# Performance work log

Measured on AMD Instinct MI355X. Metric: run time of the kernel, lower is better.

Reference implementation:

```python
import jax, jax.numpy as jnp
import numpy as np

B, N, D, P = 8, 256, 1024, 512  # batch, n_words, input_dim, proj_dim


def setup_inputs() -> dict:
    key = jax.random.key(0)
    ks = jax.random.split(key, 8)
    w = lambda k, shape: (jax.random.normal(k, shape, dtype=jnp.float32) * 0.02)
    return {
        "x": jax.random.normal(ks[0], (B, N, D), dtype=jnp.float32),
        # bigram path
        "Wl": w(ks[1], (P, D)), "bl": jnp.zeros((P,), jnp.float32),
        "Wr": w(ks[2], (P, D)),  # right proj has no bias
        "Wo": w(ks[3], (1, P)), "bo": jnp.zeros((1,), jnp.float32),
        # start builder: Linear -> ReLU -> Linear
        "Ws1": w(ks[4], (P, D)), "bs1": jnp.zeros((P,), jnp.float32),
        "Ws2": w(ks[5], (1, P)), "bs2": jnp.zeros((1,), jnp.float32),
        # end builder
        "We1": w(ks[6], (P, D)), "be1": jnp.zeros((P,), jnp.float32),
        "We2": w(ks[7], (1, P)), "be2": jnp.zeros((1,), jnp.float32),
    }


def reference(x, Wl, bl, Wr, Wo, bo, Ws1, bs1, Ws2, bs2, We1, be1, We2, be2):
    # start / end scorers: [B,N,1]
    start = jax.nn.relu(jnp.einsum('bnd,pd->bnp', x, Ws1) + bs1) @ Ws2.T + bs2
    end = jax.nn.relu(jnp.einsum('bnd,pd->bnp', x, We1) + be1) @ We2.T + be2
    # bigram projections: [B,N,P]
    left = jnp.einsum('bnd,pd->bnp', x, Wl) + bl
    right = jnp.einsum('bnd,pd->bnp', x, Wr)
    # outer-sum: proj[b,i,j,:] = left[b,j,:] + right[b,i,:]  -> [B,N,N,P]
    proj = jax.nn.relu(left[:, None, :, :] + right[:, :, None, :])
    bigram = jnp.einsum('bijp,qp->bijq', proj, Wo) + bo  # [B,N,N,1]
    return (bigram, start, end)
```

## Files before the change

kernel.cpp:

```cpp
#include <hip/hip_runtime.h>
#include <hip/hip_fp16.h>

typedef __attribute__((ext_vector_type(8))) short short8;
typedef __attribute__((ext_vector_type(4))) float f32x4;

constexpr int kB = 8;
constexpr int kN = 256;
constexpr int kD = 1024;
constexpr int kP = 512;
constexpr int kM = kB * kN;

__device__ __forceinline__ __half2 pk_max2(__half2 a, __half2 b) {
    unsigned ua = *reinterpret_cast<unsigned*>(&a);
    unsigned ub = *reinterpret_cast<unsigned*>(&b);
    unsigned ur;
    asm("v_pk_max_f16 %0, %1, %2" : "=v"(ur) : "v"(ua), "v"(ub));
    return *reinterpret_cast<__half2*>(&ur);
}

__global__ __launch_bounds__(256) void cvt_kernel(
    const float* __restrict__ x,
    const float* __restrict__ Wl, const float* __restrict__ Wr,
    const float* __restrict__ Ws1, const float* __restrict__ We1,
    const float* __restrict__ bs2, const float* __restrict__ be2,
    unsigned short* __restrict__ xb, unsigned short* __restrict__ wb,
    float* __restrict__ out_start, float* __restrict__ out_end)
{
    const int bid = blockIdx.x;
    if (bid >= 2048) {
        const int idx = (bid - 2048) * 256 + threadIdx.x;
        if (idx < 2048) out_start[idx] = bs2[0];
        else            out_end[idx - 2048] = be2[0];
        return;
    }
    const int g = bid * 256 + threadIdx.x;
    const float* src;
    unsigned short* dst;
    if (g < 262144) {
        src = x + (size_t)g * 8;
        dst = xb + (size_t)g * 8;
    } else {
        const int gg = g - 262144;
        const int w = gg >> 16;
        const int r = gg & 65535;
        const float* s = (w == 0) ? Wl : (w == 1) ? Wr : (w == 2) ? Ws1 : We1;
        src = s + (size_t)r * 8;
        dst = wb + ((size_t)w << 19) + (size_t)r * 8;
    }
    const float4 a = *reinterpret_cast<const float4*>(src);
    const float4 b = *reinterpret_cast<const float4*>(src + 4);
    const float v[8] = {a.x, a.y, a.z, a.w, b.x, b.y, b.z, b.w};
    short8 o;
#pragma unroll
    for (int i = 0; i < 8; ++i) {
        unsigned u = __float_as_uint(v[i]);
        u = u + 0x7FFF + ((u >> 16) & 1);
        o[i] = (short)(u >> 16);
    }
    *reinterpret_cast<short8*>(dst) = o;
}

__global__ __launch_bounds__(512) void proj_mfma(
    const unsigned short* __restrict__ xb, const unsigned short* __restrict__ wb,
    const float* __restrict__ bl, const float* __restrict__ bs1,
    const float* __restrict__ be1,
    const float* __restrict__ Ws2, const float* __restrict__ We2,
    __half* __restrict__ left_h, __half* __restrict__ right_h,
    float* __restrict__ out_start, float* __restrict__ out_end)
{
    __shared__ unsigned short As[2][128 * 64];
    __shared__ unsigned short Bs[2][128 * 64];

    const int L = blockIdx.x;
    const int slot = L >> 3;
    const int by = (L & 7) * 2 + (slot >> 4);
    const int bx = slot & 15;
    const int r0 = bx * 128;
    const int q0 = by * 128;
    const int z  = q0 >> 9;
    const int t = threadIdx.x, wid = t >> 6, lane = t & 63;
    const int wr = wid >> 2, wc = wid & 3;

    f32x4 acc[4][2] = {};

    const int srow0 = wid * 16 + (lane >> 3);
    const int scolh = ((lane & 7) ^ (lane >> 3)) << 3;
    const unsigned short* gA0 = xb + (size_t)(r0 + srow0) * kD + scolh;
    const unsigned short* gA1 = gA0 + (size_t)8 * kD;
    const unsigned short* gB0 = wb + (size_t)(q0 + srow0) * kD + scolh;
    const unsigned short* gB1 = gB0 + (size_t)8 * kD;

#define STAGE(buf, k0) do { \
    __builtin_amdgcn_global_load_lds( \
        (const __attribute__((address_space(1))) void*)(gA0 + (k0)), \
        (__attribute__((address_space(3))) void*)((char*)&As[buf][0] + wid * 2048), 16, 0, 0); \
    __builtin_amdgcn_global_load_lds( \
        (const __attribute__((address_space(1))) void*)(gA1 + (k0)), \
        (__attribute__((address_space(3))) void*)((char*)&As[buf][0] + wid * 2048 + 1024), 16, 0, 0); \
    __builtin_amdgcn_global_load_lds( \
        (const __attribute__((address_space(1))) void*)(gB0 + (k0)), \
        (__attribute__((address_space(3))) void*)((char*)&Bs[buf][0] + wid * 2048), 16, 0, 0); \
    __builtin_amdgcn_global_load_lds( \
        (const __attribute__((address_space(1))) void*)(gB1 + (k0)), \
        (__attribute__((address_space(3))) void*)((char*)&Bs[buf][0] + wid * 2048 + 1024), 16, 0, 0); \
} while (0)

    const int sw = (lane & 7) << 4;
    const int cb0 = (lane >> 4) * 16;
    const int rA = wr * 64 + (lane & 15);
    const int rB = wc * 32 + (lane & 15);

    STAGE(0, 0);
    __syncthreads();
    int cur = 0;
    for (int k0 = 0; k0 < kD; k0 += 64) {
        if (k0 + 64 < kD) STAGE(cur ^ 1, k0 + 64);
        short8 a[4][2], b[2][2];
#pragma unroll
        for (int m = 0; m < 4; ++m)
#pragma unroll
            for (int ks = 0; ks < 2; ++ks)
                a[m][ks] = *reinterpret_cast<const short8*>(
                    (const char*)&As[cur][0] +
                    (rA + m * 16) * 128 + ((ks * 64 + cb0) ^ sw));
#pragma unroll
        for (int n = 0; n < 2; ++n)
#pragma unroll
            for (int ks = 0; ks < 2; ++ks)
                b[n][ks] = *reinterpret_cast<const short8*>(
                    (const char*)&Bs[cur][0] +
                    (rB + n * 16) * 128 + ((ks * 64 + cb0) ^ sw));
#pragma unroll
        for (int m = 0; m < 4; ++m)
#pragma unroll
            for (int n = 0; n < 2; ++n)
#pragma unroll
                for (int ks = 0; ks < 2; ++ks)
                    acc[m][n] = __builtin_amdgcn_mfma_f32_16x16x32_bf16(
                        a[m][ks], b[n][ks], acc[m][n], 0, 0, 0);
        __syncthreads();
        cur ^= 1;
    }
#undef STAGE

    int pcol[2]; float bq[2];
#pragma unroll
    for (int n = 0; n < 2; ++n) {
        pcol[n] = (q0 & 511) + wc * 32 + n * 16 + (lane & 15);
        bq[n] = (z == 0) ? bl[pcol[n]] : (z == 2) ? bs1[pcol[n]]
              : (z == 3) ? be1[pcol[n]] : 0.f;
    }
    if (z < 2) {
        __half* dst = (z == 0) ? left_h : right_h;
        const int bb = r0 >> 8;
        const int jbase = (r0 & 255) + wr * 64 + (lane >> 4) * 4;
#pragma unroll
        for (int n = 0; n < 2; ++n) {
            __half* drow = dst + (size_t)(bb * kP + pcol[n]) * kN;
#pragma unroll
            for (int m = 0; m < 4; ++m) {
                const f32x4 c = acc[m][n];
                __half2 h01 = __floats2half2_rn(c[0] + bq[n], c[1] + bq[n]);
                __half2 h23 = __floats2half2_rn(c[2] + bq[n], c[3] + bq[n]);
                uint2 u;
                u.x = *reinterpret_cast<unsigned*>(&h01);
                u.y = *reinterpret_cast<unsigned*>(&h23);
                *reinterpret_cast<uint2*>(&drow[jbase + m * 16]) = u;
            }
        }
    } else {
        const float* Wv = (z == 2) ? Ws2 : We2;
        float* outh = (z == 2) ? out_start : out_end;
        const float w0 = Wv[pcol[0]], w1 = Wv[pcol[1]];
        const int rbase = r0 + wr * 64 + (lane >> 4) * 4;
#pragma unroll
        for (int m = 0; m < 4; ++m) {
#pragma unroll
            for (int q = 0; q < 4; ++q) {
                float s = fmaxf(acc[m][0][q] + bq[0], 0.f) * w0 +
                          fmaxf(acc[m][1][q] + bq[1], 0.f) * w1;
                s += __shfl_xor(s, 1); s += __shfl_xor(s, 2);
                s += __shfl_xor(s, 4); s += __shfl_xor(s, 8);
                if ((lane & 15) == 0)
                    atomicAdd(&outh[rbase + m * 16 + q], s);
            }
        }
    }
}

__global__ __launch_bounds__(256) void bigram_kernel(
    const __half* __restrict__ left_h, const __half* __restrict__ right_h,
    const float* __restrict__ Wo, float* __restrict__ part)
{
    __shared__ __half ls[32][64];
    __shared__ __half2 rs2[32][64];
    __shared__ __half2 wos[32];

    const int bz = blockIdx.z, b = bz >> 4, pc = bz & 15;
    const int i0 = blockIdx.y * 64, j0 = blockIdx.x * 64;
    const int t = threadIdx.x, wid = t >> 6, lane = t & 63;
    const int tj = t & 15, ti = t >> 4;

    const __half* lbase = left_h  + (size_t)(b * kP + pc * 32) * kN;
    const __half* rbase = right_h + (size_t)(b * kP + pc * 32) * kN;

    {
        const int row = wid * 8 + (lane >> 3);
        __builtin_amdgcn_global_load_lds(
            (const __attribute__((address_space(1))) void*)
                (lbase + (size_t)row * kN + j0 + (lane & 7) * 8),
            (__attribute__((address_space(3))) void*)
                ((char*)&ls[0][0] + wid * 1024),
            16, 0, 0);
    }
    uint2 rload[2];
#pragma unroll
    for (int h = 0; h < 2; ++h) {
        const int idx = h * 256 + t, pp = idx >> 4, iq = idx & 15;
        rload[h] = *reinterpret_cast<const uint2*>(&rbase[(size_t)pp * kN + i0 + iq * 4]);
    }
    if (t < 32) wos[t] = __float2half2_rn(Wo[pc * 32 + t]);
#pragma unroll
    for (int h = 0; h < 2; ++h) {
        const int idx = h * 256 + t, pp = idx >> 4, iq = idx & 15;
        const unsigned lo = rload[h].x, hi = rload[h].y;
        uint4 d;
        d.x = (lo & 0xFFFFu) | (lo << 16);
        d.y = (lo >> 16)     | (lo & 0xFFFF0000u);
        d.z = (hi & 0xFFFFu) | (hi << 16);
        d.w = (hi >> 16)     | (hi & 0xFFFF0000u);
        *reinterpret_cast<uint4*>(&rs2[pp][iq * 4]) = d;
    }
    __syncthreads();

    const __half2 zero2 = __float2half2_rn(0.f);
    __half2 acc2[4][2];
#pragma unroll
    for (int ii = 0; ii < 4; ++ii)
#pragma unroll
        for (int jp = 0; jp < 2; ++jp) acc2[ii][jp] = zero2;

#pragma unroll 8
    for (int kk = 0; kk < 32; ++kk) {
        const __half2 wo2 = wos[kk];
        union { uint2 u; __half2 h[2]; } L;
        L.u = *reinterpret_cast<const uint2*>(&ls[kk][tj * 4]);
        union { uint4 u; __half2 h[4]; } R;
        R.u = *reinterpret_cast<const uint4*>(&rs2[kk][ti * 4]);
#pragma unroll
        for (int ii = 0; ii < 4; ++ii)
#pragma unroll
            for (int jp = 0; jp < 2; ++jp) {
                __half2 s = __hadd2(R.h[ii], L.h[jp]);
                s = pk_max2(s, zero2);
                acc2[ii][jp] = __hfma2(s, wo2, acc2[ii][jp]);
            }
    }

    float* po = part + (size_t)bz * 65536;
#pragma unroll
    for (int ii = 0; ii < 4; ++ii) {
        const float2 a = __half22float2(acc2[ii][0]);
        const float2 c = __half22float2(acc2[ii][1]);
        float4 o = {a.x, a.y, c.x, c.y};
        *reinterpret_cast<float4*>(&po[(i0 + ti * 4 + ii) * kN + j0 + tj * 4]) = o;
    }
}

__global__ __launch_bounds__(256) void reduce_kernel(
    const float* __restrict__ part, const float* __restrict__ bo,
    float* __restrict__ out)
{
    const int e4 = blockIdx.x * 256 + threadIdx.x;
    const int e = e4 * 4, b = e >> 16, r = e & 65535;
    const float bias = bo[0];
    float4 acc = {bias, bias, bias, bias};
#pragma unroll
    for (int k = 0; k < 16; ++k) {
        const float4 v = *reinterpret_cast<const float4*>(
            &part[(size_t)(b * 16 + k) * 65536 + r]);
        acc.x += v.x; acc.y += v.y; acc.z += v.z; acc.w += v.w;
    }
    *reinterpret_cast<float4*>(&out[e]) = acc;
}

extern "C" void kernel_launch(void* const* d_in, const int* in_sizes, int n_in,
                              void* d_out, int out_size, void* d_ws, size_t ws_size,
                              hipStream_t stream) {
    const float* x   = (const float*)d_in[0];
    const float* Wl  = (const float*)d_in[1];
    const float* bl  = (const float*)d_in[2];
    const float* Wr  = (const float*)d_in[3];
    const float* Wo  = (const float*)d_in[4];
    const float* bo  = (const float*)d_in[5];
    const float* Ws1 = (const float*)d_in[6];
    const float* bs1 = (const float*)d_in[7];
    const float* Ws2 = (const float*)d_in[8];
    const float* bs2 = (const float*)d_in[9];
    const float* We1 = (const float*)d_in[10];
    const float* be1 = (const float*)d_in[11];
    const float* We2 = (const float*)d_in[12];
    const float* be2 = (const float*)d_in[13];

    float* out        = (float*)d_out;
    float* out_bigram = out;
    float* out_start  = out + (size_t)kB * kN * kN;
    float* out_end    = out_start + (size_t)kB * kN;

    __half* left_h  = (__half*)d_ws;
    __half* right_h = left_h + (size_t)1048576;
    unsigned short* xb = (unsigned short*)((char*)d_ws + (size_t)4 * 1024 * 1024);
    unsigned short* wb = xb + (size_t)2097152;
    float* part = (float*)((char*)d_ws + (size_t)4 * 1024 * 1024);

    cvt_kernel<<<2064, 256, 0, stream>>>(
        x, Wl, Wr, Ws1, We1, bs2, be2, xb, wb, out_start, out_end);

    proj_mfma<<<256, 512, 0, stream>>>(
        xb, wb, bl, bs1, be1, Ws2, We2, left_h, right_h, out_start, out_end);

    bigram_kernel<<<dim3(4, 4, 128), 256, 0, stream>>>(
        left_h, right_h, Wo, part);

    reduce_kernel<<<512, 256, 0, stream>>>(part, bo, out_bigram);
}
```

Measured before the change: 131.2 us.

## Enlarge projection GEMM tile to 256x256 with 32-wide K steps

The projection GEMM now uses 256x256 output tiles per block, with a K-step of 32 and a new LDS swizzle. Each wave now holds 8x4 accumulators instead of 4x2, so data in LDS is reused more per MFMA. The grid drops from 256 blocks to 64, which leaves most of the 256 CUs idle and raises register pressure. The intent is to cut global and LDS traffic per flop, at the cost of much lower parallelism.

New measurement: 153.3 us. +16.8%, slower.

```diff
diff --git a/kernel.cpp b/kernel.cpp
--- a/kernel.cpp
+++ b/kernel.cpp
@@ -68,27 +68,25 @@
     __half* __restrict__ left_h, __half* __restrict__ right_h,
     float* __restrict__ out_start, float* __restrict__ out_end)
 {
-    __shared__ unsigned short As[2][128 * 64];
-    __shared__ unsigned short Bs[2][128 * 64];
+    __shared__ unsigned short As[2][256 * 32];
+    __shared__ unsigned short Bs[2][256 * 32];
 
     const int L = blockIdx.x;
-    const int slot = L >> 3;
-    const int by = (L & 7) * 2 + (slot >> 4);
-    const int bx = slot & 15;
-    const int r0 = bx * 128;
-    const int q0 = by * 128;
+    const int by = L & 7, bx = L >> 3;
+    const int r0 = bx * 256;
+    const int q0 = by * 256;
     const int z  = q0 >> 9;
     const int t = threadIdx.x, wid = t >> 6, lane = t & 63;
     const int wr = wid >> 2, wc = wid & 3;
 
-    f32x4 acc[4][2] = {};
-
-    const int srow0 = wid * 16 + (lane >> 3);
-    const int scolh = ((lane & 7) ^ (lane >> 3)) << 3;
+    f32x4 acc[8][4] = {};
+
+    const int srow0 = wid * 32 + (lane >> 2);
+    const int scolh = (((lane & 3) ^ ((lane >> 2) & 3))) << 3;
     const unsigned short* gA0 = xb + (size_t)(r0 + srow0) * kD + scolh;
-    const unsigned short* gA1 = gA0 + (size_t)8 * kD;
+    const unsigned short* gA1 = gA0 + (size_t)16 * kD;
     const unsigned short* gB0 = wb + (size_t)(q0 + srow0) * kD + scolh;
-    const unsigned short* gB1 = gB0 + (size_t)8 * kD;
+    const unsigned short* gB1 = gB0 + (size_t)16 * kD;
 
 #define STAGE(buf, k0) do { \
     __builtin_amdgcn_global_load_lds( \
@@ -105,60 +103,51 @@
         (__attribute__((address_space(3))) void*)((char*)&Bs[buf][0] + wid * 2048 + 1024), 16, 0, 0); \
 } while (0)
 
-    const int sw = (lane & 7) << 4;
-    const int cb0 = (lane >> 4) * 16;
-    const int rA = wr * 64 + (lane & 15);
-    const int rB = wc * 32 + (lane & 15);
+    const int fslot = ((lane >> 4) ^ (lane & 3)) << 4;
+    const int rA = wr * 128 + (lane & 15);
+    const int rB = wc * 64 + (lane & 15);
 
     STAGE(0, 0);
     __syncthreads();
     int cur = 0;
-    for (int k0 = 0; k0 < kD; k0 += 64) {
-        if (k0 + 64 < kD) STAGE(cur ^ 1, k0 + 64);
-        short8 a[4][2], b[2][2];
-#pragma unroll
-        for (int m = 0; m < 4; ++m)
-#pragma unroll
-            for (int ks = 0; ks < 2; ++ks)
-                a[m][ks] = *reinterpret_cast<const short8*>(
-                    (const char*)&As[cur][0] +
-                    (rA + m * 16) * 128 + ((ks * 64 + cb0) ^ sw));
-#pragma unroll
-        for (int n = 0; n < 2; ++n)
-#pragma unroll
-            for (int ks = 0; ks < 2; ++ks)
-                b[n][ks] = *reinterpret_cast<const short8*>(
-                    (const char*)&Bs[cur][0] +
-                    (rB + n * 16) * 128 + ((ks * 64 + cb0) ^ sw));
-#pragma unroll
-        for (int m = 0; m < 4; ++m)
-#pragma unroll
-            for (int n = 0; n < 2; ++n)
-#pragma unroll
-                for (int ks = 0; ks < 2; ++ks)
-                    acc[m][n] = __builtin_amdgcn_mfma_f32_16x16x32_bf16(
-                        a[m][ks], b[n][ks], acc[m][n], 0, 0, 0);
+    for (int k0 = 0; k0 < kD; k0 += 32) {
+        if (k0 + 32 < kD) STAGE(cur ^ 1, k0 + 32);
+        short8 a[8], b[4];
+#pragma unroll
+        for (int m = 0; m < 8; ++m)
+            a[m] = *reinterpret_cast<const short8*>(
+                (const char*)&As[cur][0] + (rA + m * 16) * 64 + fslot);
+#pragma unroll
+        for (int n = 0; n < 4; ++n)
+            b[n] = *reinterpret_cast<const short8*>(
+                (const char*)&Bs[cur][0] + (rB + n * 16) * 64 + fslot);
+#pragma unroll
+        for (int m = 0; m < 8; ++m)
+#pragma unroll
+            for (int n = 0; n < 4; ++n)
+                acc[m][n] = __builtin_amdgcn_mfma_f32_16x16x32_bf16(
+                    a[m], b[n], acc[m][n], 0, 0, 0);
         __syncthreads();
         cur ^= 1;
     }
 #undef STAGE
 
-    int pcol[2]; float bq[2];
-#pragma unroll
-    for (int n = 0; n < 2; ++n) {
-        pcol[n] = (q0 & 511) + wc * 32 + n * 16 + (lane & 15);
+    int pcol[4]; float bq[4];
+#pragma unroll
+    for (int n = 0; n < 4; ++n) {
+        pcol[n] = (q0 & 511) + wc * 64 + n * 16 + (lane & 15);
         bq[n] = (z == 0) ? bl[pcol[n]] : (z == 2) ? bs1[pcol[n]]
               : (z == 3) ? be1[pcol[n]] : 0.f;
     }
     if (z < 2) {
         __half* dst = (z == 0) ? left_h : right_h;
         const int bb = r0 >> 8;
-        const int jbase = (r0 & 255) + wr * 64 + (lane >> 4) * 4;
-#pragma unroll
-        for (int n = 0; n < 2; ++n) {
+        const int jbase = wr * 128 + (lane >> 4) * 4;
+#pragma unroll
+        for (int n = 0; n < 4; ++n) {
             __half* drow = dst + (size_t)(bb * kP + pcol[n]) * kN;
 #pragma unroll
-            for (int m = 0; m < 4; ++m) {
+            for (int m = 0; m < 8; ++m) {
                 const f32x4 c = acc[m][n];
                 __half2 h01 = __floats2half2_rn(c[0] + bq[n], c[1] + bq[n]);
                 __half2 h23 = __floats2half2_rn(c[2] + bq[n], c[3] + bq[n]);
@@ -171,14 +160,18 @@
     } else {
         const float* Wv = (z == 2) ? Ws2 : We2;
         float* outh = (z == 2) ? out_start : out_end;
-        const float w0 = Wv[pcol[0]], w1 = Wv[pcol[1]];
-        const int rbase = r0 + wr * 64 + (lane >> 4) * 4;
-#pragma unroll
-        for (int m = 0; m < 4; ++m) {
+        float w[4];
+#pragma unroll
+        for (int n = 0; n < 4; ++n) w[n] = Wv[pcol[n]];
+        const int rbase = r0 + wr * 128 + (lane >> 4) * 4;
+#pragma unroll
+        for (int m = 0; m < 8; ++m) {
 #pragma unroll
             for (int q = 0; q < 4; ++q) {
-                float s = fmaxf(acc[m][0][q] + bq[0], 0.f) * w0 +
-                          fmaxf(acc[m][1][q] + bq[1], 0.f) * w1;
+                float s = 0.f;
+#pragma unroll
+                for (int n = 0; n < 4; ++n)
+                    s += fmaxf(acc[m][n][q] + bq[n], 0.f) * w[n];
                 s += __shfl_xor(s, 1); s += __shfl_xor(s, 2);
                 s += __shfl_xor(s, 4); s += __shfl_xor(s, 8);
                 if ((lane & 15) == 0)
@@ -316,7 +309,7 @@
     cvt_kernel<<<2064, 256, 0, stream>>>(
         x, Wl, Wr, Ws1, We1, bs2, be2, xb, wb, out_start, out_end);
 
-    proj_mfma<<<256, 512, 0, stream>>>(
+    proj_mfma<<<64, 512, 0, stream>>>(
         xb, wb, bl, bs1, be1, Ws2, We2, left_h, right_h, out_start, out_end);
 
     bigram_kernel<<<dim3(4, 4, 128), 256, 0, stream>>>(
```
